# Kernel tuning notes

Hardware: AMD Instinct MI355X
Metric: run time of the kernel (lower is better)

Reference implementation:

```python
import jax, jax.numpy as jnp
import numpy as np

NH, L, P, HD = 8, 3, 8, 32  # nhead, num_levels, num_points, head_dim
C = NH * HD                 # d_model = 256


def setup_inputs() -> dict:
    key = jax.random.key(0)
    ks = jax.random.split(key, 10)
    B, Nq = 4, 2048
    # 3-level feature pyramid: 100x100, 50x50, 25x25 -> S = 13125
    spatial_shapes = np.array([[100, 100], [50, 50], [25, 25]], dtype=np.int64)
    level_start_index = np.array([0, 10000, 12500], dtype=np.int64)
    S = 13125
    inv_sqrt_c = 1.0 / np.sqrt(C).astype(np.float32)
    return {
        "query": jax.random.normal(ks[0], (B, Nq, C), jnp.float32),
        "memory": jax.random.normal(ks[1], (B, S, C), jnp.float32),
        "reference_points": jax.random.uniform(ks[2], (B, Nq, 2), jnp.float32),
        "W_off": jax.random.normal(ks[3], (C, NH * L * P * 2), jnp.float32) * 0.01,
        "b_off": jax.random.normal(ks[4], (NH * L * P * 2,), jnp.float32),
        "W_attn": jax.random.normal(ks[5], (C, NH * L * P), jnp.float32) * 0.02,
        "b_attn": jnp.zeros((NH * L * P,), jnp.float32),
        "W_val": jax.random.normal(ks[6], (C, C), jnp.float32) * inv_sqrt_c,
        "b_val": jnp.zeros((C,), jnp.float32),
        "W_out": jax.random.normal(ks[7], (C, C), jnp.float32) * inv_sqrt_c,
        "b_out": jnp.zeros((C,), jnp.float32),
        "spatial_shapes": spatial_shapes,
        "level_start_index": level_start_index,
    }


def _bilinear(vl, gx, gy, h, w):
    """grid_sample(mode=bilinear, padding_mode=zeros, align_corners=False).
    vl: [B, NH, H*W, D] level features; gx, gy: [B, NH, N] grid coords in [-1, 1].
    Returns [B, NH, N, D]."""
    x = ((gx + 1.0) * w - 1.0) * 0.5
    y = ((gy + 1.0) * h - 1.0) * 0.5
    x0 = jnp.floor(x)
    y0 = jnp.floor(y)
    acc = 0.0
    corners = (
        (x0,       y0,       (x0 + 1.0 - x) * (y0 + 1.0 - y)),
        (x0 + 1.0, y0,       (x - x0) * (y0 + 1.0 - y)),
        (x0,       y0 + 1.0, (x0 + 1.0 - x) * (y - y0)),
        (x0 + 1.0, y0 + 1.0, (x - x0) * (y - y0)),
    )
    for xi, yi, wt in corners:
        valid = (xi >= 0) & (xi < w) & (yi >= 0) & (yi < h)
        xc = jnp.clip(xi, 0, w - 1).astype(jnp.int32)
        yc = jnp.clip(yi, 0, h - 1).astype(jnp.int32)
        idx = (yc * w + xc)[..., None]                      # [B, NH, N, 1]
        v = jnp.take_along_axis(vl, idx, axis=2)            # [B, NH, N, D]
        acc = acc + v * (wt * valid.astype(wt.dtype))[..., None]
    return acc


def _forward(query, memory, reference_points, W_off, b_off, W_attn, b_attn,
             W_val, b_val, W_out, b_out, ss, lsi):
    B, Nq, _ = query.shape
    S = memory.shape[1]
    # value projection -> [B, NH, S, HD]
    value = (memory @ W_val + b_val).reshape(B, S, NH, HD).transpose(0, 2, 1, 3)
    off = (query @ W_off + b_off).reshape(B, Nq, NH, L, P, 2)
    attn = jax.nn.softmax((query @ W_attn + b_attn).reshape(B, Nq, NH, L * P), axis=-1)
    attn = attn.reshape(B, Nq, NH, L, P)
    # per-level (w, h) normalizer
    norm = jnp.asarray(np.stack([ss[:, 1], ss[:, 0]], axis=-1), jnp.float32)  # [L, 2]
    loc = reference_points[:, :, None, None, None, :] + off / norm[None, None, None, :, None, :]
    grid = loc * 2.0 - 1.0                                   # [B, Nq, NH, L, P, 2]
    out = jnp.zeros((B, Nq, NH, HD), query.dtype)
    for level in range(L):
        h, w = int(ss[level, 0]), int(ss[level, 1])
        start = int(lsi[level])
        vl = value[:, :, start:start + h * w, :]             # [B, NH, h*w, HD]
        g = jnp.transpose(grid[:, :, :, level], (0, 2, 1, 3, 4)).reshape(B, NH, Nq * P, 2)
        sampled = _bilinear(vl, g[..., 0], g[..., 1], h, w).reshape(B, NH, Nq, P, HD)
        out = out + jnp.einsum('bhqpd,bqhp->bqhd', sampled, attn[:, :, :, level])
    return out.reshape(B, Nq, NH * HD) @ W_out + b_out


def reference(query, memory, reference_points, W_off, b_off, W_attn, b_attn,
              W_val, b_val, W_out, b_out, spatial_shapes, level_start_index):
    ss = np.asarray(spatial_shapes)
    lsi = np.asarray(level_start_index)
    return _forward(query, memory, reference_points, W_off, b_off, W_attn, b_attn,
                    W_val, b_val, W_out, b_out, ss, lsi)
```

## Files before the change

kernel.cpp:

```cpp
#include <hip/hip_runtime.h>
#include <math.h>

#define NH_ 8
#define L_ 3
#define P_ 8
#define HD_ 32
#define C_ 256
#define B_ 4
#define NQ 2048
#define S_ 13125

typedef unsigned short ushort;
typedef unsigned int uint;

__device__ __constant__ const int kLW[3]     = {100, 50, 25};
__device__ __constant__ const int kLH[3]     = {100, 50, 25};
__device__ __constant__ const int kLSTART[3] = {0, 10000, 12500};

using short8 = __attribute__((ext_vector_type(8))) short;
using f32x4  = __attribute__((ext_vector_type(4))) float;

typedef unsigned int u32_as1 __attribute__((address_space(1)));
typedef unsigned int u32_as3 __attribute__((address_space(3)));

__device__ __forceinline__ void gload16(const ushort* g, ushort* l) {
    __builtin_amdgcn_global_load_lds((const u32_as1*)g, (u32_as3*)l, 16, 0, 0);
}

__device__ __forceinline__ ushort f2bf(float f) {
    union { float f; uint i; } v; v.f = f;
    const uint x = v.i;
    return (ushort)((x + 0x7FFFu + ((x >> 16) & 1u)) >> 16);
}
__device__ __forceinline__ float bf2f(ushort u) {
    union { uint i; float f; } v; v.i = ((uint)u) << 16; return v.f;
}
__device__ __forceinline__ uint pk2(float lo, float hi) {
    return (uint)f2bf(lo) | ((uint)f2bf(hi) << 16);
}

__global__ __launch_bounds__(256) void convert_kernel(
    const float* __restrict__ memory, const float* __restrict__ query,
    const float* __restrict__ W_off, const float* __restrict__ W_attn,
    const float* __restrict__ W_val, const float* __restrict__ W_out,
    ushort* __restrict__ memB, ushort* __restrict__ queryB,
    ushort* __restrict__ WcatT, ushort* __restrict__ W_valT,
    ushort* __restrict__ W_outT)
{
    const uint id = blockIdx.x * 256u + threadIdx.x;
    if (id < 1680000u) {
        const float4 a = *(const float4*)(memory + (size_t)id * 8);
        const float4 b = *(const float4*)(memory + (size_t)id * 8 + 4);
        uint4 o; o.x = pk2(a.x, a.y); o.y = pk2(a.z, a.w);
                 o.z = pk2(b.x, b.y); o.w = pk2(b.z, b.w);
        *(uint4*)(memB + (size_t)id * 8) = o;
    } else if (id < 1942144u) {
        const uint i = id - 1680000u;
        const float4 a = *(const float4*)(query + (size_t)i * 8);
        const float4 b = *(const float4*)(query + (size_t)i * 8 + 4);
        uint4 o; o.x = pk2(a.x, a.y); o.y = pk2(a.z, a.w);
                 o.z = pk2(b.x, b.y); o.w = pk2(b.z, b.w);
        *(uint4*)(queryB + (size_t)i * 8) = o;
    } else if (id < 2007680u) {
        const uint i = id - 1942144u;
        const uint n = i >> 8, k = i & 255u;
        W_valT[i] = f2bf(W_val[k * 256 + n]);
    } else if (id < 2155136u) {
        const uint i = id - 2007680u;
        const uint n = i >> 8, k = i & 255u;
        WcatT[i] = f2bf(n < 384u ? W_off[k * 384 + n] : W_attn[k * 192 + (n - 384)]);
    } else if (id < 2220672u) {
        const uint i = id - 2155136u;
        const uint n = i >> 8, k = i & 255u;
        W_outT[i] = f2bf(W_out[k * 256 + n]);
    }
}

template <int MODE>
__global__ __launch_bounds__(256) void gemm_mfma(
    const ushort* __restrict__ A, const ushort* __restrict__ WT,
    const float* __restrict__ bias1, const float* __restrict__ bias2,
    void* __restrict__ outp)
{
    const int tid = threadIdx.x;
    const int wid = tid >> 6, lane = tid & 63;
    const int l15 = lane & 15, kcl = lane >> 4;
    const int wr = wid >> 1, wc = wid & 1;

    int M, N;
    const ushort* Ab;
    if constexpr (MODE == 0) { M = S_;  N = 256; Ab = A + (size_t)blockIdx.z * S_ * 256; }
    else if constexpr (MODE == 1) { M = 8192; N = 576; Ab = A; }
    else { M = 8192; N = 256; Ab = A; }

    const int row0 = blockIdx.x * 128, n0 = blockIdx.y * 128;

    __shared__ ushort As[2][4096];
    __shared__ ushort Bs[2][4096];

    f32x4 acc[4][4] = {};

    auto stage = [&](int buf, int k0) {
        #pragma unroll
        for (int rh = 0; rh < 2; ++rh) {
            int r = row0 + rh * 64 + lane;
            if (MODE == 0) r = min(r, M - 1);
            gload16(Ab + (size_t)r * 256 + k0 + wid * 8,
                    &As[buf][wid * 1024 + rh * 512]);
            int c = n0 + rh * 64 + lane;
            if (MODE == 1) c = min(c, N - 1);
            gload16(WT + (size_t)c * 256 + k0 + wid * 8,
                    &Bs[buf][wid * 1024 + rh * 512]);
        }
    };

    stage(0, 0);
    __syncthreads();

    #pragma unroll
    for (int kt = 0; kt < 8; ++kt) {
        const int cur = kt & 1;
        if (kt < 7) stage(cur ^ 1, (kt + 1) * 32);

        short8 af[4], bf[4];
        #pragma unroll
        for (int mi = 0; mi < 4; ++mi)
            af[mi] = *(const short8*)&As[cur][kcl * 1024 + (wr * 64 + mi * 16 + l15) * 8];
        #pragma unroll
        for (int ni = 0; ni < 4; ++ni)
            bf[ni] = *(const short8*)&Bs[cur][kcl * 1024 + (wc * 64 + ni * 16 + l15) * 8];
        #pragma unroll
        for (int mi = 0; mi < 4; ++mi)
            #pragma unroll
            for (int ni = 0; ni < 4; ++ni)
                acc[mi][ni] = __builtin_amdgcn_mfma_f32_16x16x32_bf16(
                    af[mi], bf[ni], acc[mi][ni], 0, 0, 0);
        __syncthreads();
    }

    #pragma unroll
    for (int ni = 0; ni < 4; ++ni) {
        const int n = n0 + wc * 64 + ni * 16 + l15;
        if constexpr (MODE == 0) {
            ushort* value = (ushort*)outp;
            const int h = n >> 5, d = n & 31;
            const float bv = bias1[n];
            #pragma unroll
            for (int mi = 0; mi < 4; ++mi)
                #pragma unroll
                for (int r = 0; r < 4; ++r) {
                    const int s = row0 + wr * 64 + mi * 16 + kcl * 4 + r;
                    if (s < S_)
                        value[(((size_t)blockIdx.z * NH_ + h) * S_ + s) * HD_ + d] =
                            f2bf(acc[mi][ni][r] + bv);
                }
        } else if constexpr (MODE == 1) {
            if (n < 576) {
                float* o = (float*)outp;
                const float bv = (n < 384) ? bias1[n] : bias2[n - 384];
                #pragma unroll
                for (int mi = 0; mi < 4; ++mi)
                    #pragma unroll
                    for (int r = 0; r < 4; ++r) {
                        const int gr = row0 + wr * 64 + mi * 16 + kcl * 4 + r;
                        o[(size_t)gr * 576 + n] = acc[mi][ni][r] + bv;
                    }
            }
        } else {
            float* o = (float*)outp;
            const float bv = bias1[n];
            #pragma unroll
            for (int mi = 0; mi < 4; ++mi)
                #pragma unroll
                for (int r = 0; r < 4; ++r) {
                    const int gr = row0 + wr * 64 + mi * 16 + kcl * 4 + r;
                    o[(size_t)gr * 256 + n] = acc[mi][ni][r] + bv;
                }
        }
    }
}

__global__ __launch_bounds__(256, 8) void sample_kernel(
    const ushort* __restrict__ value,
    const float*  __restrict__ projQ,
    const float*  __restrict__ refp,
    ushort* __restrict__ out_preB)
{
    const int wib  = threadIdx.x >> 6;
    const int lane = threadIdx.x & 63;
    const int half = lane >> 5, dl = lane & 31;

    const int bid = blockIdx.x;
    const int swz = (bid & 7) * 2048 + (bid >> 3);
    const int bh = swz >> 9;
    const int q  = ((swz & 511) << 2) + wib;
    const int b  = bh >> 3, h = bh & 7;
    const int row = b * NQ + q;

    const float* lg = projQ + (size_t)row * 576 + 384 + h * 24 + half;
    float l[12];
    float m = -1e30f;
    #pragma unroll
    for (int j = 0; j < 12; ++j) { l[j] = lg[2 * j]; m = fmaxf(m, l[j]); }
    m = fmaxf(m, __shfl_xor(m, 32));
    float s = 0.f;
    #pragma unroll
    for (int j = 0; j < 12; ++j) { l[j] = __expf(l[j] - m); s += l[j]; }
    s += __shfl_xor(s, 32);
    const float inv = 1.0f / s;

    const float refx = refp[(size_t)row * 2 + 0];
    const float refy = refp[(size_t)row * 2 + 1];
    const float* off = projQ + (size_t)row * 576 + h * 48 + half * 2;

    const uint vbh = (uint)(b * NH_ + h) * (uint)(S_ * HD_);
    float acc = 0.f;
    #pragma unroll
    for (int it = 0; it < 12; ++it) {
        const int lvl = it >> 2;
        const int w = kLW[lvl], hh = kLH[lvl];
        const uint vbase = vbh + (uint)kLSTART[lvl] * HD_ + dl;

        const float ox = off[it * 4 + 0];
        const float oy = off[it * 4 + 1];
        const float x = fmaf(refx, (float)w,  ox) - 0.5f;
        const float y = fmaf(refy, (float)hh, oy) - 0.5f;
        const float x0f = floorf(x), y0f = floorf(y);
        const float fx = x - x0f, fy = y - y0f;
        const int ix = (int)x0f, iy = (int)y0f;

        const float cx0 = (ix >= 0 && ix < w)         ? (1.f - fx) : 0.f;
        const float cx1 = (ix + 1 >= 0 && ix + 1 < w) ? fx         : 0.f;
        const float cy0 = (iy >= 0 && iy < hh)         ? (1.f - fy) : 0.f;
        const float cy1 = (iy + 1 >= 0 && iy + 1 < hh) ? fy         : 0.f;
        const int xc0 = min(max(ix, 0), w - 1),  xc1 = min(max(ix + 1, 0), w - 1);
        const int yc0 = min(max(iy, 0), hh - 1), yc1 = min(max(iy + 1, 0), hh - 1);

        const uint r0 = vbase + (uint)(yc0 * w) * HD_;
        const uint r1 = vbase + (uint)(yc1 * w) * HD_;
        const float v00 = bf2f(value[r0 + (uint)xc0 * HD_]);
        const float v10 = bf2f(value[r0 + (uint)xc1 * HD_]);
        const float v01 = bf2f(value[r1 + (uint)xc0 * HD_]);
        const float v11 = bf2f(value[r1 + (uint)xc1 * HD_]);

        const float sv = cy0 * (cx0 * v00 + cx1 * v10) + cy1 * (cx0 * v01 + cx1 * v11);
        acc = fmaf(l[it] * inv, sv, acc);
    }

    acc += __shfl_xor(acc, 32);
    if (half == 0)
        out_preB[(size_t)row * 256 + h * HD_ + dl] = f2bf(acc);
}

extern "C" void kernel_launch(void* const* d_in, const int* in_sizes, int n_in,
                              void* d_out, int out_size, void* d_ws, size_t ws_size,
                              hipStream_t stream)
{
    const float* query  = (const float*)d_in[0];
    const float* memory = (const float*)d_in[1];
    const float* refp   = (const float*)d_in[2];
    const float* W_off  = (const float*)d_in[3];
    const float* b_off  = (const float*)d_in[4];
    const float* W_attn = (const float*)d_in[5];
    const float* b_attn = (const float*)d_in[6];
    const float* W_val  = (const float*)d_in[7];
    const float* b_val  = (const float*)d_in[8];
    const float* W_out  = (const float*)d_in[9];
    const float* b_out  = (const float*)d_in[10];

    ushort* ws       = (ushort*)d_ws;
    ushort* memB     = ws;
    ushort* queryB   = memB + 13440000;
    ushort* W_valT   = queryB + 2097152;
    ushort* WcatT    = W_valT + 65536;
    ushort* W_outT   = WcatT + 147456;
    ushort* valueB   = W_outT + 65536;
    float*  projQ    = (float*)memB;
    ushort* out_preB = memB + 9437184;

    hipLaunchKernelGGL(convert_kernel, dim3(8675), dim3(256), 0, stream,
                       memory, query, W_off, W_attn, W_val, W_out,
                       memB, queryB, WcatT, W_valT, W_outT);
    hipLaunchKernelGGL((gemm_mfma<0>), dim3(103, 2, 4), dim3(256), 0, stream,
                       memB, W_valT, b_val, nullptr, (void*)valueB);
    hipLaunchKernelGGL((gemm_mfma<1>), dim3(64, 5, 1), dim3(256), 0, stream,
                       queryB, WcatT, b_off, b_attn, (void*)projQ);
    hipLaunchKernelGGL(sample_kernel, dim3(16384), dim3(256), 0, stream,
                       valueB, projQ, refp, out_preB);
    hipLaunchKernelGGL((gemm_mfma<2>), dim3(64, 2, 1), dim3(256), 0, stream,
                       out_preB, W_outT, b_out, nullptr, (void*)d_out);
}
```

Before: 246.6 us.

## Pre-tile GEMM operands into LDS-ready layout and parallelize sampling setup across lanes

The convert kernel now writes memory, query and the transposed weights in a tile-blocked layout that matches the LDS staging pattern, so GEMM staging becomes contiguous loads with no row clamping. Weight transposes are vectorized to eight elements per thread. The sample kernel now computes each sampling point's coordinates, softmax and bilinear weights once per lane, then broadcasts offsets and weights with shuffles, so the 12-iteration loop is reduced to gathers. It also writes its output in the tiled layout the output GEMM expects. This couples the layouts of all the kernels together, and the strided weight reads in the convert kernel are less coalesced.

```diff
diff --git a/kernel.cpp b/kernel.cpp
--- a/kernel.cpp
+++ b/kernel.cpp
@@ -12,10 +12,6 @@
 
 typedef unsigned short ushort;
 typedef unsigned int uint;
-
-__device__ __constant__ const int kLW[3]     = {100, 50, 25};
-__device__ __constant__ const int kLH[3]     = {100, 50, 25};
-__device__ __constant__ const int kLSTART[3] = {0, 10000, 12500};
 
 using short8 = __attribute__((ext_vector_type(8))) short;
 using f32x4  = __attribute__((ext_vector_type(4))) float;
@@ -48,31 +44,67 @@
     ushort* __restrict__ W_outT)
 {
     const uint id = blockIdx.x * 256u + threadIdx.x;
-    if (id < 1680000u) {
-        const float4 a = *(const float4*)(memory + (size_t)id * 8);
-        const float4 b = *(const float4*)(memory + (size_t)id * 8 + 4);
+    float v[8];
+
+    if (id < 1687552u) {
+        const uint z = id / 421888u, rem = id % 421888u;
+        const uint t = rem >> 12, c = rem & 4095u;
+        const uint s = c >> 9, w = (c >> 7) & 3u, rh = (c >> 6) & 1u, ln = c & 63u;
+        const uint r = min(t * 128u + rh * 64u + ln, 13124u);
+        const uint k = s * 32u + w * 8u;
+        const float* src = memory + ((size_t)z * 13125u + r) * 256u + k;
+        const float4 a = *(const float4*)src;
+        const float4 b = *(const float4*)(src + 4);
         uint4 o; o.x = pk2(a.x, a.y); o.y = pk2(a.z, a.w);
                  o.z = pk2(b.x, b.y); o.w = pk2(b.z, b.w);
         *(uint4*)(memB + (size_t)id * 8) = o;
-    } else if (id < 1942144u) {
-        const uint i = id - 1680000u;
-        const float4 a = *(const float4*)(query + (size_t)i * 8);
-        const float4 b = *(const float4*)(query + (size_t)i * 8 + 4);
+    } else if (id < 1949696u) {
+        const uint local = id - 1687552u;
+        const uint t = local >> 12, c = local & 4095u;
+        const uint s = c >> 9, w = (c >> 7) & 3u, rh = (c >> 6) & 1u, ln = c & 63u;
+        const uint r = t * 128u + rh * 64u + ln;
+        const uint k = s * 32u + w * 8u;
+        const float* src = query + (size_t)r * 256u + k;
+        const float4 a = *(const float4*)src;
+        const float4 b = *(const float4*)(src + 4);
         uint4 o; o.x = pk2(a.x, a.y); o.y = pk2(a.z, a.w);
                  o.z = pk2(b.x, b.y); o.w = pk2(b.z, b.w);
-        *(uint4*)(queryB + (size_t)i * 8) = o;
-    } else if (id < 2007680u) {
-        const uint i = id - 1942144u;
-        const uint n = i >> 8, k = i & 255u;
-        W_valT[i] = f2bf(W_val[k * 256 + n]);
-    } else if (id < 2155136u) {
-        const uint i = id - 2007680u;
-        const uint n = i >> 8, k = i & 255u;
-        WcatT[i] = f2bf(n < 384u ? W_off[k * 384 + n] : W_attn[k * 192 + (n - 384)]);
-    } else if (id < 2220672u) {
-        const uint i = id - 2155136u;
-        const uint n = i >> 8, k = i & 255u;
-        W_outT[i] = f2bf(W_out[k * 256 + n]);
+        *(uint4*)(queryB + (size_t)local * 8) = o;
+    } else if (id < 1957888u) {
+        const uint local = id - 1949696u;
+        const uint t = local >> 12, c = local & 4095u;
+        const uint s = c >> 9, w = (c >> 7) & 3u, rh = (c >> 6) & 1u, ln = c & 63u;
+        const uint n = t * 128u + rh * 64u + ln;
+        const uint k = s * 32u + w * 8u;
+        #pragma unroll
+        for (int e = 0; e < 8; ++e) v[e] = W_val[(size_t)(k + e) * 256u + n];
+        uint4 o; o.x = pk2(v[0], v[1]); o.y = pk2(v[2], v[3]);
+                 o.z = pk2(v[4], v[5]); o.w = pk2(v[6], v[7]);
+        *(uint4*)(W_valT + (size_t)local * 8) = o;
+    } else if (id < 1978368u) {
+        const uint local = id - 1957888u;
+        const uint t = local >> 12, c = local & 4095u;
+        const uint s = c >> 9, w = (c >> 7) & 3u, rh = (c >> 6) & 1u, ln = c & 63u;
+        const uint n = min(t * 128u + rh * 64u + ln, 575u);
+        const uint k = s * 32u + w * 8u;
+        #pragma unroll
+        for (int e = 0; e < 8; ++e)
+            v[e] = (n < 384u) ? W_off[(size_t)(k + e) * 384u + n]
+                              : W_attn[(size_t)(k + e) * 192u + (n - 384u)];
+        uint4 o; o.x = pk2(v[0], v[1]); o.y = pk2(v[2], v[3]);
+                 o.z = pk2(v[4], v[5]); o.w = pk2(v[6], v[7]);
+        *(uint4*)(WcatT + (size_t)local * 8) = o;
+    } else if (id < 1986560u) {
+        const uint local = id - 1978368u;
+        const uint t = local >> 12, c = local & 4095u;
+        const uint s = c >> 9, w = (c >> 7) & 3u, rh = (c >> 6) & 1u, ln = c & 63u;
+        const uint n = t * 128u + rh * 64u + ln;
+        const uint k = s * 32u + w * 8u;
+        #pragma unroll
+        for (int e = 0; e < 8; ++e) v[e] = W_out[(size_t)(k + e) * 256u + n];
+        uint4 o; o.x = pk2(v[0], v[1]); o.y = pk2(v[2], v[3]);
+                 o.z = pk2(v[4], v[5]); o.w = pk2(v[6], v[7]);
+        *(uint4*)(W_outT + (size_t)local * 8) = o;
     }
 }
 
@@ -87,11 +119,9 @@
     const int l15 = lane & 15, kcl = lane >> 4;
     const int wr = wid >> 1, wc = wid & 1;
 
-    int M, N;
     const ushort* Ab;
-    if constexpr (MODE == 0) { M = S_;  N = 256; Ab = A + (size_t)blockIdx.z * S_ * 256; }
-    else if constexpr (MODE == 1) { M = 8192; N = 576; Ab = A; }
-    else { M = 8192; N = 256; Ab = A; }
+    if constexpr (MODE == 0) Ab = A + (size_t)blockIdx.z * 3375104u;
+    else                     Ab = A;
 
     const int row0 = blockIdx.x * 128, n0 = blockIdx.y * 128;
 
@@ -100,17 +130,13 @@
 
     f32x4 acc[4][4] = {};
 
-    auto stage = [&](int buf, int k0) {
+    auto stage = [&](int buf, int s) {
+        const size_t abase = ((size_t)(blockIdx.x * 8 + s)) * 4096 + wid * 1024 + lane * 8;
+        const size_t bbase = ((size_t)(blockIdx.y * 8 + s)) * 4096 + wid * 1024 + lane * 8;
         #pragma unroll
         for (int rh = 0; rh < 2; ++rh) {
-            int r = row0 + rh * 64 + lane;
-            if (MODE == 0) r = min(r, M - 1);
-            gload16(Ab + (size_t)r * 256 + k0 + wid * 8,
-                    &As[buf][wid * 1024 + rh * 512]);
-            int c = n0 + rh * 64 + lane;
-            if (MODE == 1) c = min(c, N - 1);
-            gload16(WT + (size_t)c * 256 + k0 + wid * 8,
-                    &Bs[buf][wid * 1024 + rh * 512]);
+            gload16(Ab + abase + rh * 512, &As[buf][wid * 1024 + rh * 512]);
+            gload16(WT + bbase + rh * 512, &Bs[buf][wid * 1024 + rh * 512]);
         }
     };
 
@@ -120,7 +146,7 @@
     #pragma unroll
     for (int kt = 0; kt < 8; ++kt) {
         const int cur = kt & 1;
-        if (kt < 7) stage(cur ^ 1, (kt + 1) * 32);
+        if (kt < 7) stage(cur ^ 1, kt + 1);
 
         short8 af[4], bf[4];
         #pragma unroll
@@ -189,6 +215,8 @@
     const int wib  = threadIdx.x >> 6;
     const int lane = threadIdx.x & 63;
     const int half = lane >> 5, dl = lane & 31;
+    const int j = lane & 31;
+    const int jc = min(j, 23);
 
     const int bid = blockIdx.x;
     const int swz = (bid & 7) * 2048 + (bid >> 3);
@@ -196,60 +224,67 @@
     const int q  = ((swz & 511) << 2) + wib;
     const int b  = bh >> 3, h = bh & 7;
     const int row = b * NQ + q;
-
-    const float* lg = projQ + (size_t)row * 576 + 384 + h * 24 + half;
-    float l[12];
-    float m = -1e30f;
-    #pragma unroll
-    for (int j = 0; j < 12; ++j) { l[j] = lg[2 * j]; m = fmaxf(m, l[j]); }
-    m = fmaxf(m, __shfl_xor(m, 32));
-    float s = 0.f;
-    #pragma unroll
-    for (int j = 0; j < 12; ++j) { l[j] = __expf(l[j] - m); s += l[j]; }
-    s += __shfl_xor(s, 32);
-    const float inv = 1.0f / s;
-
+    const float* rowQ = projQ + (size_t)row * 576;
+
+    const float2 offj = *(const float2*)(rowQ + h * 48 + jc * 2);
+    const float lg = rowQ[384 + h * 24 + jc];
     const float refx = refp[(size_t)row * 2 + 0];
     const float refy = refp[(size_t)row * 2 + 1];
-    const float* off = projQ + (size_t)row * 576 + h * 48 + half * 2;
-
-    const uint vbh = (uint)(b * NH_ + h) * (uint)(S_ * HD_);
+
+    const int   wi = j < 8 ? 100 : (j < 16 ? 50 : 25);
+    const int   st = j < 8 ? 0   : (j < 16 ? 10000 : 12500);
+    const float wf = (float)wi;
+
+    const float x = fmaf(refx, wf, offj.x) - 0.5f;
+    const float y = fmaf(refy, wf, offj.y) - 0.5f;
+    const float x0f = floorf(x), y0f = floorf(y);
+    const float fx = x - x0f, fy = y - y0f;
+    const int ix = (int)x0f, iy = (int)y0f;
+
+    const float cx0 = (ix >= 0 && ix < wi)         ? (1.f - fx) : 0.f;
+    const float cx1 = (ix + 1 >= 0 && ix + 1 < wi) ? fx         : 0.f;
+    const float cy0 = (iy >= 0 && iy < wi)         ? (1.f - fy) : 0.f;
+    const float cy1 = (iy + 1 >= 0 && iy + 1 < wi) ? fy         : 0.f;
+    const int xc0 = min(max(ix, 0), wi - 1),  xc1 = min(max(ix + 1, 0), wi - 1);
+    const int yc0 = min(max(iy, 0), wi - 1),  yc1 = min(max(iy + 1, 0), wi - 1);
+
+    float mm = (j < 24) ? lg : -1e30f;
+    #pragma unroll
+    for (int d = 1; d < 32; d <<= 1) mm = fmaxf(mm, __shfl_xor(mm, d));
+    float ex = (j < 24) ? __expf(lg - mm) : 0.f;
+    float ssum = ex;
+    #pragma unroll
+    for (int d = 1; d < 32; d <<= 1) ssum += __shfl_xor(ssum, d);
+    const float aw = ex * (1.0f / ssum);
+
+    const float ww00 = aw * cy0 * cx0, ww10 = aw * cy0 * cx1;
+    const float ww01 = aw * cy1 * cx0, ww11 = aw * cy1 * cx1;
+    const uint o00 = (uint)(st + yc0 * wi + xc0) * 32u;
+    const uint o10 = (uint)(st + yc0 * wi + xc1) * 32u;
+    const uint o01 = (uint)(st + yc1 * wi + xc0) * 32u;
+    const uint o11 = (uint)(st + yc1 * wi + xc1) * 32u;
+
+    const ushort* slab = value + (size_t)(b * NH_ + h) * (S_ * HD_) + dl;
     float acc = 0.f;
     #pragma unroll
-    for (int it = 0; it < 12; ++it) {
-        const int lvl = it >> 2;
-        const int w = kLW[lvl], hh = kLH[lvl];
-        const uint vbase = vbh + (uint)kLSTART[lvl] * HD_ + dl;
-
-        const float ox = off[it * 4 + 0];
-        const float oy = off[it * 4 + 1];
-        const float x = fmaf(refx, (float)w,  ox) - 0.5f;
-        const float y = fmaf(refy, (float)hh, oy) - 0.5f;
-        const float x0f = floorf(x), y0f = floorf(y);
-        const float fx = x - x0f, fy = y - y0f;
-        const int ix = (int)x0f, iy = (int)y0f;
-
-        const float cx0 = (ix >= 0 && ix < w)         ? (1.f - fx) : 0.f;
-        const float cx1 = (ix + 1 >= 0 && ix + 1 < w) ? fx         : 0.f;
-        const float cy0 = (iy >= 0 && iy < hh)         ? (1.f - fy) : 0.f;
-        const float cy1 = (iy + 1 >= 0 && iy + 1 < hh) ? fy         : 0.f;
-        const int xc0 = min(max(ix, 0), w - 1),  xc1 = min(max(ix + 1, 0), w - 1);
-        const int yc0 = min(max(iy, 0), hh - 1), yc1 = min(max(iy + 1, 0), hh - 1);
-
-        const uint r0 = vbase + (uint)(yc0 * w) * HD_;
-        const uint r1 = vbase + (uint)(yc1 * w) * HD_;
-        const float v00 = bf2f(value[r0 + (uint)xc0 * HD_]);
-        const float v10 = bf2f(value[r0 + (uint)xc1 * HD_]);
-        const float v01 = bf2f(value[r1 + (uint)xc0 * HD_]);
-        const float v11 = bf2f(value[r1 + (uint)xc1 * HD_]);
-
-        const float sv = cy0 * (cx0 * v00 + cx1 * v10) + cy1 * (cx0 * v01 + cx1 * v11);
-        acc = fmaf(l[it] * inv, sv, acc);
-    }
-
+    for (int i = 0; i < 12; ++i) {
+        const int src = 2 * i + half;
+        const uint a00 = (uint)__shfl((int)o00, src), a10 = (uint)__shfl((int)o10, src);
+        const uint a01 = (uint)__shfl((int)o01, src), a11 = (uint)__shfl((int)o11, src);
+        const float u00 = __shfl(ww00, src), u10 = __shfl(ww10, src);
+        const float u01 = __shfl(ww01, src), u11 = __shfl(ww11, src);
+        acc = fmaf(u00, bf2f(slab[a00]), acc);
+        acc = fmaf(u10, bf2f(slab[a10]), acc);
+        acc = fmaf(u01, bf2f(slab[a01]), acc);
+        acc = fmaf(u11, bf2f(slab[a11]), acc);
+    }
     acc += __shfl_xor(acc, 32);
-    if (half == 0)
-        out_preB[(size_t)row * 256 + h * HD_ + dl] = f2bf(acc);
+    if (half == 0) {
+        const uint toff = ((uint)(row >> 7)) * 32768u + (uint)h * 4096u
+                        + (uint)(dl >> 3) * 1024u + (uint)((row >> 6) & 1) * 512u
+                        + (uint)(row & 63) * 8u + (uint)(dl & 7);
+        out_preB[toff] = f2bf(acc);
+    }
 }
 
 extern "C" void kernel_launch(void* const* d_in, const int* in_sizes, int n_in,
@@ -270,15 +305,15 @@
 
     ushort* ws       = (ushort*)d_ws;
     ushort* memB     = ws;
-    ushort* queryB   = memB + 13440000;
-    ushort* W_valT   = queryB + 2097152;
-    ushort* WcatT    = W_valT + 65536;
-    ushort* W_outT   = WcatT + 147456;
-    ushort* valueB   = W_outT + 65536;
-    float*  projQ    = (float*)memB;
-    ushort* out_preB = memB + 9437184;
-
-    hipLaunchKernelGGL(convert_kernel, dim3(8675), dim3(256), 0, stream,
+    ushort* queryB   = ws + 13500416;
+    ushort* W_valT   = ws + 15597568;
+    ushort* WcatT    = ws + 15663104;
+    ushort* W_outT   = ws + 15826944;
+    ushort* valueB   = ws + 15892480;
+    float*  projQ    = (float*)ws;
+    ushort* out_preB = ws + 9437184;
+
+    hipLaunchKernelGGL(convert_kernel, dim3(7760), dim3(256), 0, stream,
                        memory, query, W_off, W_attn, W_val, W_out,
                        memB, queryB, WcatT, W_valT, W_outT);
     hipLaunchKernelGGL((gemm_mfma<0>), dim3(103, 2, 4), dim3(256), 0, stream,
```

New measurement: 257.8 us. 4.6% more time.
